# Kernel optimization log

Measured on AMD Instinct MI355X. Metric: run time of the kernel, lower is better.

## Reference

```python
import jax, jax.numpy as jnp
import numpy as np
import math

B, T, C, F = 8, 2048, 1024, 4096
N_LAYER, LAYER_ID = 12, 1


def _init_params(key):
    ks = jax.random.split(key, 16)
    s = 0.02
    ratio_0_to_1 = LAYER_ID / (N_LAYER - 1)
    ratio_1_to_almost0 = 1.0 - LAYER_ID / N_LAYER
    h = np.arange(C, dtype=np.float32)
    decay = -5.0 + 8.0 * (h / (C - 1)) ** (0.7 + 1.3 * ratio_0_to_1)
    zigzag = np.array([((i + 1) % 3 - 1) for i in range(C)], dtype=np.float32) * 0.5
    first = np.ones(C, dtype=np.float32) * math.log(0.3) + zigzag
    xi = (np.arange(C, dtype=np.float32) / C)
    p = {
        'ln1_w': jnp.ones(C), 'ln1_b': jnp.zeros(C),
        'ln2_w': jnp.ones(C), 'ln2_b': jnp.zeros(C),
        'att_time_decay': jnp.asarray(decay),
        'att_time_first': jnp.asarray(first),
        'att_mix_k': jnp.asarray(xi ** ratio_1_to_almost0),
        'att_mix_v': jnp.asarray(xi ** ratio_1_to_almost0 + 0.3 * ratio_0_to_1),
        'att_mix_r': jnp.asarray(xi ** (0.5 * ratio_1_to_almost0)),
        'att_Wk': jax.random.normal(ks[0], (C, C)) * s,
        'att_Wv': jax.random.normal(ks[1], (C, C)) * s,
        'att_Wr': jax.random.normal(ks[2], (C, C)) * s,
        'att_Wo': jax.random.normal(ks[3], (C, C)) * s,
        'ffn_mix_k': jnp.asarray(xi ** ratio_1_to_almost0),
        'ffn_mix_r': jnp.asarray(xi ** ratio_1_to_almost0),
        'ffn_Wk': jax.random.normal(ks[4], (F, C)) * s,
        'ffn_Wr': jax.random.normal(ks[5], (C, C)) * s,
        'ffn_Wv': jax.random.normal(ks[6], (C, F)) * s,
        'short_W': jax.random.normal(ks[7], (C, C)) * s,
    }
    return p


def setup_inputs() -> dict:
    key = jax.random.key(0)
    k1, k2 = jax.random.split(key)
    inp = {'x': jax.random.normal(k1, (B, T, C), dtype=jnp.float32)}
    inp.update(_init_params(k2))
    return inp


def _layernorm(x, w, b, eps=1e-5):
    mu = jnp.mean(x, axis=-1, keepdims=True)
    var = jnp.var(x, axis=-1, keepdims=True)
    return (x - mu) * jax.lax.rsqrt(var + eps) * w + b


def _time_shift(x):
    # ZeroPad2d((0,0,1,-1)): prepend zero row along T, drop last
    return jnp.pad(x, ((0, 0), (1, 0), (0, 0)))[:, :-1]


def _wkv(time_decay, time_first, k, v):
    # numerically-stable WKV recurrence, matching the CUDA kernel math
    w = -jnp.exp(time_decay)  # [C]
    u = time_first            # [C]
    kt = jnp.swapaxes(k, 0, 1)  # [T,B,C]
    vt = jnp.swapaxes(v, 0, 1)
    a0 = jnp.zeros(k.shape[::2] if False else (k.shape[0], k.shape[2]), k.dtype)
    b0 = jnp.zeros_like(a0)
    p0 = jnp.full_like(a0, -1e30)

    def step(carry, kv):
        a, b, p = carry
        k_t, v_t = kv
        ww = u + k_t
        q = jnp.maximum(p, ww)
        e1 = jnp.exp(p - q)
        e2 = jnp.exp(ww - q)
        y = (e1 * a + e2 * v_t) / (e1 * b + e2)
        ww2 = p + w
        q2 = jnp.maximum(ww2, k_t)
        f1 = jnp.exp(ww2 - q2)
        f2 = jnp.exp(k_t - q2)
        return (f1 * a + f2 * v_t, f1 * b + f2, q2), y

    _, ys = jax.lax.scan(step, (a0, b0, p0), (kt, vt))
    return jnp.swapaxes(ys, 0, 1)  # [B,T,C]


def _lin(x, W):
    return jnp.einsum('btc,oc->bto', x, W)


def reference(x, ln1_w, ln1_b, ln2_w, ln2_b,
              att_time_decay, att_time_first, att_mix_k, att_mix_v, att_mix_r,
              att_Wk, att_Wv, att_Wr, att_Wo,
              ffn_mix_k, ffn_mix_r, ffn_Wk, ffn_Wr, ffn_Wv, short_W):
    # --- TimeMix on ln1(x) ---
    h = _layernorm(x, ln1_w, ln1_b)
    hh = _time_shift(h)
    xk = h * att_mix_k + hh * (1 - att_mix_k)
    xv = h * att_mix_v + hh * (1 - att_mix_v)
    xr = h * att_mix_r + hh * (1 - att_mix_r)
    k = _lin(xk, att_Wk)
    v = _lin(xv, att_Wv)
    sr = jax.nn.sigmoid(_lin(xr, att_Wr))
    rwkv = sr * _wkv(att_time_decay, att_time_first, k, v)
    att_out = _lin(rwkv, att_Wo)
    # shortcut linear replaces identity residual (L3TC Block)
    x = _lin(x, short_W) + att_out
    # --- ChannelMix on ln2(x) ---
    g = _layernorm(x, ln2_w, ln2_b)
    gg = _time_shift(g)
    gk = g * ffn_mix_k + gg * (1 - ffn_mix_k)
    gr = g * ffn_mix_r + gg * (1 - ffn_mix_r)
    kk = jnp.square(jax.nn.relu(_lin(gk, ffn_Wk)))
    kv = _lin(kk, ffn_Wv)
    rkv = jax.nn.sigmoid(_lin(gr, ffn_Wr)) * kv
    return x + rkv
```

## Files before the change

### kernel.cpp

```cpp
#include <hip/hip_runtime.h>

#define BB 8
#define TT 2048
#define CC 1024
#define FF 4096
#define MM (BB*TT)

typedef unsigned short u16;
typedef __bf16 bf16x8 __attribute__((ext_vector_type(8)));
typedef float f32x4 __attribute__((ext_vector_type(4)));

__device__ __forceinline__ u16 f2bf(float f) {
  unsigned int u = __float_as_uint(f);
  u += 0x7fffu + ((u >> 16) & 1u);
  return (u16)(u >> 16);
}
__device__ __forceinline__ float bf2f(u16 h) {
  unsigned int u = ((unsigned int)h) << 16;
  return __uint_as_float(u);
}
__device__ __forceinline__ float sigm(float x) { return 1.f / (1.f + __expf(-x)); }

__device__ __forceinline__ void async16(const void* g, void* l) {
  __builtin_amdgcn_global_load_lds(
      (const __attribute__((address_space(1))) unsigned int*)g,
      (__attribute__((address_space(3))) unsigned int*)l, 16, 0, 0);
}

#define GROUP_M 16

template<int MODE>
__device__ __forceinline__ void gemm_body(
    const u16* __restrict__ A, const u16* __restrict__ W,
    float* __restrict__ Cf, u16* __restrict__ Cb,
    const u16* __restrict__ R, int N, int K)
{
  __shared__ __align__(16) u16 ldsA[128 * 32];
  __shared__ __align__(16) u16 ldsB[128 * 32];
  const int tid  = threadIdx.x;
  const int wave = tid >> 6;
  const int lane = tid & 63;

  const int bid  = blockIdx.x + blockIdx.y * gridDim.x;
  const int gsz  = GROUP_M * gridDim.y;
  const int gid  = bid / gsz;
  const int rem  = bid - gid * gsz;
  const int bm   = (gid * GROUP_M + (rem % GROUP_M)) * 128;
  const int bn   = (rem / GROUP_M) * 128;

  const int wm = (wave >> 1) * 64;
  const int wn = (wave & 1) * 64;
  const int lm = lane & 15;
  const int lq = lane >> 4;

  const int r_in = lane >> 2;
  const int cp   = lane & 3;
  const int cg   = cp ^ ((r_in >> 1) & 3);
  const int rA0  = wave * 16 + r_in;
  const int rA1  = 64 + rA0;
  const u16* gA0 = A + (size_t)(bm + rA0) * K + cg * 8;
  const u16* gA1 = A + (size_t)(bm + rA1) * K + cg * 8;
  const u16* gB0 = W + (size_t)(bn + rA0) * K + cg * 8;
  const u16* gB1 = W + (size_t)(bn + rA1) * K + cg * 8;
  u16* lA0 = &ldsA[(wave * 16) * 32];
  u16* lA1 = &ldsA[(64 + wave * 16) * 32];
  u16* lB0 = &ldsB[(wave * 16) * 32];
  u16* lB1 = &ldsB[(64 + wave * 16) * 32];

  const int crd  = lq ^ ((lm >> 1) & 3);
  const int offA0 = (wm + lm) * 32 + crd * 8;
  const int offB0 = (wn + lm) * 32 + crd * 8;

  f32x4 acc[4][4] = {};

  for (int kt = 0; kt < K; kt += 32) {
    async16(gA0 + kt, lA0);
    async16(gA1 + kt, lA1);
    async16(gB0 + kt, lB0);
    async16(gB1 + kt, lB1);
    __syncthreads();
    bf16x8 bfr[4];
#pragma unroll
    for (int ni = 0; ni < 4; ++ni)
      bfr[ni] = *(const bf16x8*)&ldsB[offB0 + ni * 16 * 32];
#pragma unroll
    for (int mi = 0; mi < 4; ++mi) {
      bf16x8 afr = *(const bf16x8*)&ldsA[offA0 + mi * 16 * 32];
#pragma unroll
      for (int ni = 0; ni < 4; ++ni)
        acc[mi][ni] = __builtin_amdgcn_mfma_f32_16x16x32_bf16(afr, bfr[ni], acc[mi][ni], 0, 0, 0);
    }
    __syncthreads();
  }

  const int row0 = bm + wm + lq * 4;
  const int col0 = bn + wn + lm;
#pragma unroll
  for (int mi = 0; mi < 4; ++mi)
#pragma unroll
    for (int ni = 0; ni < 4; ++ni) {
      size_t base = (size_t)(row0 + mi * 16) * N + (col0 + ni * 16);
#pragma unroll
      for (int r2 = 0; r2 < 4; ++r2) {
        size_t idx = base + (size_t)r2 * N;
        float v = acc[mi][ni][r2];
        if (MODE == 0) Cf[idx] = v;
        if (MODE == 2) { float rl = v > 0.f ? v : 0.f; Cb[idx] = f2bf(rl * rl); }
        if (MODE == 3) Cb[idx] = f2bf(v);
        if (MODE == 4) Cf[idx] += sigm(bf2f(R[idx])) * v;
      }
    }
}

template<int MODE>
__global__ __launch_bounds__(256, 2) void gemm_bt(
    const u16* __restrict__ A, const u16* __restrict__ W,
    float* __restrict__ Cf, u16* __restrict__ Cb,
    const u16* __restrict__ R, int N, int K)
{
  gemm_body<MODE>(A, W, Cf, Cb, R, N, K);
}

__global__ __launch_bounds__(256) void prep_mix(
    const float* __restrict__ x,
    const float* __restrict__ lnw, const float* __restrict__ lnb,
    const float* __restrict__ mk, const float* __restrict__ mv, const float* __restrict__ mr,
    u16* __restrict__ ok, u16* __restrict__ ov, u16* __restrict__ orr,
    u16* __restrict__ oxb)
{
  const int m = blockIdx.x;
  const int t = m & (TT - 1);
  const int tid = threadIdx.x;
  const int wave = tid >> 6, lane = tid & 63;
  const bool hasp = (t != 0);

  const float4 xc4 = ((const float4*)(x + (size_t)m * CC))[tid];
  float4 xp4 = make_float4(0.f, 0.f, 0.f, 0.f);
  if (hasp) xp4 = ((const float4*)(x + (size_t)(m - 1) * CC))[tid];

  float s0 = xc4.x + xc4.y + xc4.z + xc4.w;
  float s1 = xc4.x*xc4.x + xc4.y*xc4.y + xc4.z*xc4.z + xc4.w*xc4.w;
  float s2 = xp4.x + xp4.y + xp4.z + xp4.w;
  float s3 = xp4.x*xp4.x + xp4.y*xp4.y + xp4.z*xp4.z + xp4.w*xp4.w;
#pragma unroll
  for (int off2 = 32; off2 > 0; off2 >>= 1) {
    s0 += __shfl_xor(s0, off2);
    s1 += __shfl_xor(s1, off2);
    s2 += __shfl_xor(s2, off2);
    s3 += __shfl_xor(s3, off2);
  }
  __shared__ float red[4][4];
  if (lane == 0) { red[0][wave] = s0; red[1][wave] = s1; red[2][wave] = s2; red[3][wave] = s3; }
  __syncthreads();
  const float S0 = red[0][0] + red[0][1] + red[0][2] + red[0][3];
  const float S1 = red[1][0] + red[1][1] + red[1][2] + red[1][3];
  const float S2 = red[2][0] + red[2][1] + red[2][2] + red[2][3];
  const float S3 = red[3][0] + red[3][1] + red[3][2] + red[3][3];
  const float inv = 1.f / (float)CC;
  const float muc = S0 * inv, varc = S1 * inv - muc * muc, rsc = rsqrtf(varc + 1e-5f);
  const float mup = S2 * inv, varp = S3 * inv - mup * mup, rsp = rsqrtf(varp + 1e-5f);

  const float xc[4] = {xc4.x, xc4.y, xc4.z, xc4.w};
  const float xp[4] = {xp4.x, xp4.y, xp4.z, xp4.w};
  const float4 lw4 = ((const float4*)lnw)[tid];
  const float4 lb4 = ((const float4*)lnb)[tid];
  const float lw[4] = {lw4.x, lw4.y, lw4.z, lw4.w};
  const float lb[4] = {lb4.x, lb4.y, lb4.z, lb4.w};
  const float4 mk4 = ((const float4*)mk)[tid];
  const float mka[4] = {mk4.x, mk4.y, mk4.z, mk4.w};
  const float4 mr4 = ((const float4*)mr)[tid];
  const float mra[4] = {mr4.x, mr4.y, mr4.z, mr4.w};
  float mva[4] = {0.f, 0.f, 0.f, 0.f};
  if (ov) {
    const float4 mv4 = ((const float4*)mv)[tid];
    mva[0] = mv4.x; mva[1] = mv4.y; mva[2] = mv4.z; mva[3] = mv4.w;
  }

  ushort4 wk2, wv2, wr2, wb2;
  u16* pk = (u16*)&wk2; u16* pv = (u16*)&wv2; u16* pr = (u16*)&wr2; u16* pb = (u16*)&wb2;
#pragma unroll
  for (int j = 0; j < 4; ++j) {
    float h  = (xc[j] - muc) * rsc * lw[j] + lb[j];
    float hh = hasp ? (xp[j] - mup) * rsp * lw[j] + lb[j] : 0.f;
    pk[j] = f2bf(h * mka[j] + hh * (1.f - mka[j]));
    pv[j] = f2bf(h * mva[j] + hh * (1.f - mva[j]));
    pr[j] = f2bf(h * mra[j] + hh * (1.f - mra[j]));
    pb[j] = f2bf(xc[j]);
  }
  ((ushort4*)(ok + (size_t)m * CC))[tid] = wk2;
  if (ov)  ((ushort4*)(ov  + (size_t)m * CC))[tid] = wv2;
  ((ushort4*)(orr + (size_t)m * CC))[tid] = wr2;
  if (oxb) ((ushort4*)(oxb + (size_t)m * (2 * CC)))[tid] = wb2;
}

#define WKV_CPB 32
#define WKV_NCH 32
#define WKV_L   (TT / WKV_NCH)

__global__ __launch_bounds__(1024) void wkv_scan(
    const u16* __restrict__ k, const u16* __restrict__ v, const u16* __restrict__ r,
    const float* __restrict__ decay, const float* __restrict__ first,
    u16* __restrict__ out)
{
  const int b  = blockIdx.x >> 5;
  const int c0 = (blockIdx.x & 31) * WKV_CPB;
  const int tid = threadIdx.x;
  const int cl = tid & 31;
  const int j  = tid >> 5;
  const int c  = c0 + cl;

  const float w   = -__expf(decay[c]);
  const float lam = __expf(w);
  const float eu  = __expf(first[c]);

  const size_t base  = (size_t)b * TT * CC + (size_t)j * WKV_L * CC + c;
  size_t obase = ((size_t)b * TT + (size_t)j * WKV_L) * (2 * CC) + c;

  float a = 0.f, bb = 0.f;
  size_t idx = base;
  for (int i = 0; i < WKV_L; ++i, idx += CC) {
    const float kt = bf2f(k[idx]), vt = bf2f(v[idx]);
    const float ek = __expf(kt);
    a  = fmaf(lam, a, ek * vt);
    bb = fmaf(lam, bb, ek);
  }

  __shared__ float sA[WKV_NCH][WKV_CPB];
  __shared__ float sB[WKV_NCH][WKV_CPB];
  sA[j][cl] = a; sB[j][cl] = bb;
  __syncthreads();
  if (tid < WKV_CPB) {
    float ca = 0.f, cb = 0.f;
    const float cw   = -__expf(decay[c0 + tid]);
    const float cLam = __expf(cw * (float)WKV_L);
#pragma unroll
    for (int q = 0; q < WKV_NCH; ++q) {
      const float ta = sA[q][tid], tb = sB[q][tid];
      sA[q][tid] = ca; sB[q][tid] = cb;
      ca = fmaf(cLam, ca, ta);
      cb = fmaf(cLam, cb, tb);
    }
  }
  __syncthreads();
  a = sA[j][cl]; bb = sB[j][cl];

  idx = base;
  for (int i = 0; i < WKV_L; ++i, idx += CC, obase += 2 * CC) {
    const float kt = bf2f(k[idx]), vt = bf2f(v[idx]), rt = bf2f(r[idx]);
    const float ek = __expf(kt);
    const float e2 = eu * ek;
    const float y  = (a + e2 * vt) / (bb + e2);
    out[obase] = f2bf(sigm(rt) * y);
    a  = fmaf(lam, a, ek * vt);
    bb = fmaf(lam, bb, ek);
  }
}

struct ConvArgs { const float* src[8]; int end[8]; int dstoff[8]; };

__global__ __launch_bounds__(256) void conv_w(ConvArgs args, u16* __restrict__ dst)
{
  const int i = (blockIdx.x * 256 + threadIdx.x) * 4;
  int seg = 0;
  const float* sp = args.src[0];
  int base = 0;
#pragma unroll
  for (int s = 1; s < 8; ++s) {
    if (i >= args.end[s - 1]) { seg = s; sp = args.src[s]; base = args.end[s - 1]; }
  }
  const int l = i - base;
  const float4 vv = *(const float4*)(sp + l);
  int dsti;
  if (seg == 3)      { int row = l >> 10, col = l & 1023; dsti = args.dstoff[3] + row * 2048 + 1024 + col; }
  else if (seg == 4) { int row = l >> 10, col = l & 1023; dsti = args.dstoff[4] + row * 2048 + col; }
  else               dsti = args.dstoff[seg] + l;
  ushort4 d;
  d.x = f2bf(vv.x); d.y = f2bf(vv.y); d.z = f2bf(vv.z); d.w = f2bf(vv.w);
  *(ushort4*)(dst + dsti) = d;
}

extern "C" void kernel_launch(void* const* d_in, const int* in_sizes, int n_in,
                              void* d_out, int out_size, void* d_ws, size_t ws_size,
                              hipStream_t stream)
{
  const float* x    = (const float*)d_in[0];
  const float* ln1w = (const float*)d_in[1];
  const float* ln1b = (const float*)d_in[2];
  const float* ln2w = (const float*)d_in[3];
  const float* ln2b = (const float*)d_in[4];
  const float* tdec = (const float*)d_in[5];
  const float* tfir = (const float*)d_in[6];
  const float* amk  = (const float*)d_in[7];
  const float* amv  = (const float*)d_in[8];
  const float* amr  = (const float*)d_in[9];
  const float* Wk   = (const float*)d_in[10];
  const float* Wv   = (const float*)d_in[11];
  const float* Wr   = (const float*)d_in[12];
  const float* Wo   = (const float*)d_in[13];
  const float* fmk  = (const float*)d_in[14];
  const float* fmr  = (const float*)d_in[15];
  const float* WfK  = (const float*)d_in[16];
  const float* WfR  = (const float*)d_in[17];
  const float* WfV  = (const float*)d_in[18];
  const float* Wsh  = (const float*)d_in[19];
  float* out = (float*)d_out;
  char* ws = (char*)d_ws;

  u16* wW = (u16*)(ws);
  u16* U0 = (u16*)(ws + 29360128);
  u16* U1 = (u16*)(ws + 62914560);
  u16* U2 = (u16*)(ws + 96468992);
  u16* U3 = (u16*)(ws + 130023424);
  u16* U4 = (u16*)(ws + 163577856);

  u16* xk   = U0;
  u16* xv   = U1;
  u16* xr   = U2;
  u16* Ap   = U4;
  u16* kbuf = U3;
  u16* vbuf = U0;
  u16* rbuf = U1;
  u16* gk   = U0;
  u16* gr   = U1;
  u16* kkb  = U2;
  u16* rffn = U0;

  u16* bWk   = wW + 0;
  u16* bWv   = wW + 1048576;
  u16* bWr   = wW + 2097152;
  u16* bWsWo = wW + 3145728;
  u16* bWfR  = wW + 5242880;
  u16* bWfK  = wW + 6291456;
  u16* bWfV  = wW + 10485760;

  ConvArgs ca;
  ca.src[0] = Wk;  ca.src[1] = Wv;  ca.src[2] = Wr;  ca.src[3] = Wo;
  ca.src[4] = Wsh; ca.src[5] = WfR; ca.src[6] = WfK; ca.src[7] = WfV;
  const int e = 1048576;
  ca.end[0] = e;     ca.end[1] = 2*e;  ca.end[2] = 3*e;  ca.end[3] = 4*e;
  ca.end[4] = 5*e;   ca.end[5] = 6*e;  ca.end[6] = 10*e; ca.end[7] = 14*e;
  ca.dstoff[0] = 0;     ca.dstoff[1] = e;    ca.dstoff[2] = 2*e;
  ca.dstoff[3] = 3*e;   ca.dstoff[4] = 3*e;
  ca.dstoff[5] = 5*e;   ca.dstoff[6] = 6*e;  ca.dstoff[7] = 10*e;

  conv_w<<<14336, 256, 0, stream>>>(ca, wW);
  prep_mix<<<MM, 256, 0, stream>>>(x, ln1w, ln1b, amk, amv, amr, xk, xv, xr, Ap);

  dim3 g8(MM / 128, CC / 128);
  gemm_bt<3><<<g8, 256, 0, stream>>>(xk, bWk, nullptr, kbuf, nullptr, CC, CC);
  gemm_bt<3><<<g8, 256, 0, stream>>>(xv, bWv, nullptr, vbuf, nullptr, CC, CC);
  gemm_bt<3><<<g8, 256, 0, stream>>>(xr, bWr, nullptr, rbuf, nullptr, CC, CC);

  wkv_scan<<<BB * (CC / WKV_CPB), 1024, 0, stream>>>(kbuf, vbuf, rbuf, tdec, tfir, Ap + CC);

  gemm_bt<0><<<g8, 256, 0, stream>>>(Ap, bWsWo, out, nullptr, nullptr, CC, 2 * CC);

  prep_mix<<<MM, 256, 0, stream>>>(out, ln2w, ln2b, fmk, nullptr, fmr, gk, nullptr, gr, nullptr);

  dim3 gF(MM / 128, FF / 128);
  gemm_bt<2><<<gF, 256, 0, stream>>>(gk, bWfK, nullptr, kkb, nullptr, FF, CC);
  gemm_bt<3><<<g8, 256, 0, stream>>>(gr, bWfR, nullptr, rffn, nullptr, CC, CC);
  gemm_bt<4><<<g8, 256, 0, stream>>>(kkb, bWfV, out, nullptr, rffn, CC, FF);
}
```

Baseline: 887.9 us.

## Switch GEMM to 32x32x16 MFMA with K-tile 64 and new LDS layout

Replaces the 16x16x32 bf16 MFMA tiling with 32x32x16 MFMA instructions, giving each wave a 2x2 grid of 32x32 accumulators. The K step per iteration doubles to 64, which halves the number of barrier pairs, and the LDS tiles are re-laid out so each lane's fragment is a contiguous 16-byte chunk. The epilogue index mapping is rewritten to match the 32x32 accumulator layout. LDS use doubles, which may affect occupancy, and the new layout drops the XOR swizzle, so bank conflicts are possible.

```diff
diff --git a/kernel.cpp b/kernel.cpp
--- a/kernel.cpp
+++ b/kernel.cpp
@@ -8,7 +8,7 @@
 
 typedef unsigned short u16;
 typedef __bf16 bf16x8 __attribute__((ext_vector_type(8)));
-typedef float f32x4 __attribute__((ext_vector_type(4)));
+typedef float f32x16 __attribute__((ext_vector_type(16)));
 
 __device__ __forceinline__ u16 f2bf(float f) {
   unsigned int u = __float_as_uint(f);
@@ -35,8 +35,8 @@
     float* __restrict__ Cf, u16* __restrict__ Cb,
     const u16* __restrict__ R, int N, int K)
 {
-  __shared__ __align__(16) u16 ldsA[128 * 32];
-  __shared__ __align__(16) u16 ldsB[128 * 32];
+  __shared__ __align__(16) u16 ldsA[128 * 64];
+  __shared__ __align__(16) u16 ldsB[128 * 64];
   const int tid  = threadIdx.x;
   const int wave = tid >> 6;
   const int lane = tid & 63;
@@ -50,60 +50,56 @@
 
   const int wm = (wave >> 1) * 64;
   const int wn = (wave & 1) * 64;
-  const int lm = lane & 15;
-  const int lq = lane >> 4;
-
-  const int r_in = lane >> 2;
-  const int cp   = lane & 3;
-  const int cg   = cp ^ ((r_in >> 1) & 3);
-  const int rA0  = wave * 16 + r_in;
-  const int rA1  = 64 + rA0;
-  const u16* gA0 = A + (size_t)(bm + rA0) * K + cg * 8;
-  const u16* gA1 = A + (size_t)(bm + rA1) * K + cg * 8;
-  const u16* gB0 = W + (size_t)(bn + rA0) * K + cg * 8;
-  const u16* gB1 = W + (size_t)(bn + rA1) * K + cg * 8;
-  u16* lA0 = &ldsA[(wave * 16) * 32];
-  u16* lA1 = &ldsA[(64 + wave * 16) * 32];
-  u16* lB0 = &ldsB[(wave * 16) * 32];
-  u16* lB1 = &ldsB[(64 + wave * 16) * 32];
-
-  const int crd  = lq ^ ((lm >> 1) & 3);
-  const int offA0 = (wm + lm) * 32 + crd * 8;
-  const int offB0 = (wn + lm) * 32 + crd * 8;
-
-  f32x4 acc[4][4] = {};
-
-  for (int kt = 0; kt < K; kt += 32) {
-    async16(gA0 + kt, lA0);
-    async16(gA1 + kt, lA1);
-    async16(gB0 + kt, lB0);
-    async16(gB1 + kt, lB1);
+  const int l31 = lane & 31;
+  const int l5  = lane >> 5;
+
+  const int cA = 2 * wave + l5;
+  const u16* gAp[4]; const u16* gBp[4];
+  u16* lAp[4]; u16* lBp[4];
+#pragma unroll
+  for (int g = 0; g < 4; ++g) {
+    gAp[g] = A + (size_t)(bm + g * 32 + l31) * K + cA * 8;
+    gBp[g] = W + (size_t)(bn + g * 32 + l31) * K + cA * 8;
+    lAp[g] = &ldsA[g * 2048 + wave * 512 + lane * 8];
+    lBp[g] = &ldsB[g * 2048 + wave * 512 + lane * 8];
+  }
+
+  const int aoff = (wm >> 5) * 2048 + lane * 8;
+  const int boff = (wn >> 5) * 2048 + lane * 8;
+
+  f32x16 acc[2][2] = {};
+
+  for (int kt = 0; kt < K; kt += 64) {
+#pragma unroll
+    for (int g = 0; g < 4; ++g) async16(gAp[g] + kt, lAp[g]);
+#pragma unroll
+    for (int g = 0; g < 4; ++g) async16(gBp[g] + kt, lBp[g]);
     __syncthreads();
-    bf16x8 bfr[4];
-#pragma unroll
-    for (int ni = 0; ni < 4; ++ni)
-      bfr[ni] = *(const bf16x8*)&ldsB[offB0 + ni * 16 * 32];
-#pragma unroll
-    for (int mi = 0; mi < 4; ++mi) {
-      bf16x8 afr = *(const bf16x8*)&ldsA[offA0 + mi * 16 * 32];
-#pragma unroll
-      for (int ni = 0; ni < 4; ++ni)
-        acc[mi][ni] = __builtin_amdgcn_mfma_f32_16x16x32_bf16(afr, bfr[ni], acc[mi][ni], 0, 0, 0);
+#pragma unroll
+    for (int t = 0; t < 4; ++t) {
+      bf16x8 a0 = *(const bf16x8*)&ldsA[aoff + t * 512];
+      bf16x8 a1 = *(const bf16x8*)&ldsA[aoff + 2048 + t * 512];
+      bf16x8 b0 = *(const bf16x8*)&ldsB[boff + t * 512];
+      bf16x8 b1 = *(const bf16x8*)&ldsB[boff + 2048 + t * 512];
+      acc[0][0] = __builtin_amdgcn_mfma_f32_32x32x16_bf16(a0, b0, acc[0][0], 0, 0, 0);
+      acc[0][1] = __builtin_amdgcn_mfma_f32_32x32x16_bf16(a0, b1, acc[0][1], 0, 0, 0);
+      acc[1][0] = __builtin_amdgcn_mfma_f32_32x32x16_bf16(a1, b0, acc[1][0], 0, 0, 0);
+      acc[1][1] = __builtin_amdgcn_mfma_f32_32x32x16_bf16(a1, b1, acc[1][1], 0, 0, 0);
     }
     __syncthreads();
   }
 
-  const int row0 = bm + wm + lq * 4;
-  const int col0 = bn + wn + lm;
-#pragma unroll
-  for (int mi = 0; mi < 4; ++mi)
-#pragma unroll
-    for (int ni = 0; ni < 4; ++ni) {
-      size_t base = (size_t)(row0 + mi * 16) * N + (col0 + ni * 16);
-#pragma unroll
-      for (int r2 = 0; r2 < 4; ++r2) {
-        size_t idx = base + (size_t)r2 * N;
-        float v = acc[mi][ni][r2];
+  const int row00 = bm + wm + 4 * l5;
+  const int col00 = bn + wn + l31;
+#pragma unroll
+  for (int mi = 0; mi < 2; ++mi)
+#pragma unroll
+    for (int ni = 0; ni < 2; ++ni) {
+#pragma unroll
+      for (int r = 0; r < 16; ++r) {
+        const int row = row00 + mi * 32 + (r & 3) + 8 * (r >> 2);
+        const size_t idx = (size_t)row * N + (col00 + ni * 32);
+        const float v = acc[mi][ni][r];
         if (MODE == 0) Cf[idx] = v;
         if (MODE == 2) { float rl = v > 0.f ? v : 0.f; Cb[idx] = f2bf(rl * rl); }
         if (MODE == 3) Cb[idx] = f2bf(v);
```

Result: slower. 1.220 ms (+37.4%).
